# Kernel tuning notes

Hardware: AMD Instinct MI355X
Metric: run time of the kernel (lower is better)

## Reference

```python
import jax, jax.numpy as jnp
import numpy as np

DN = ('NCHW', 'OIHW', 'NCHW')

def _conv(x, w, b=None):
    # x: [P, C, H, W], w: [1, C, k, k] -> [P, 1, H, W] with SAME padding
    y = jax.lax.conv_general_dilated(x, w, (1, 1), 'SAME', dimension_numbers=DN)
    if b is not None:
        y = y + b[None, :, None, None]
    return y

def setup_inputs() -> dict:
    key = jax.random.key(0)
    ks = jax.random.split(key, 6)
    T, P, H, W = 36, 64, 128, 256
    K = 5
    inputs = jax.random.normal(ks[0], (T, P, H, W), dtype=jnp.float32)
    w_reset = 0.1 * jax.random.normal(ks[1], (1, 2, K, K), dtype=jnp.float32)
    b_reset = jnp.zeros((1,), dtype=jnp.float32)
    w_update = 0.1 * jax.random.normal(ks[2], (1, 2, K, K), dtype=jnp.float32)
    b_update = jnp.zeros((1,), dtype=jnp.float32)
    w_out = 0.1 * jax.random.normal(ks[3], (1, 2, K, K), dtype=jnp.float32)
    gam = jnp.ones((P,), dtype=jnp.float32)
    add_weights = 0.02 * jax.random.normal(ks[4], (P, H, W), dtype=jnp.float32)
    bias = jnp.zeros((H, W), dtype=jnp.float32)
    return {"inputs": inputs, "w_reset": w_reset, "b_reset": b_reset,
            "w_update": w_update, "b_update": b_update, "w_out": w_out,
            "gam": gam, "add_weights": add_weights, "bias": bias}

def reference(inputs, w_reset, b_reset, w_update, b_update, w_out, gam, add_weights, bias):
    # inputs: [T, P, H, W]; renormalize by per-plant scale gam
    x = gam[None, :, None, None] * inputs
    x = x[:, :, None]  # [T, P, 1, H, W] (channel dim = 1)
    h0 = jnp.zeros_like(x[0])  # [P, 1, H, W]

    def step(h, xt):
        stacked = jnp.concatenate([xt, h], axis=1)  # [P, 2, H, W]
        u = jax.nn.sigmoid(_conv(stacked, w_update, b_update))  # update gate
        r = jax.nn.sigmoid(_conv(stacked, w_reset, b_reset))    # reset gate
        c = _conv(jnp.concatenate([xt, r * h], axis=1), w_out)  # candidate (no bias, no act)
        h_new = h * (1.0 - u) + c * u
        return h_new, h_new

    _, states = jax.lax.scan(step, h0, x)  # [T, P, 1, H, W]
    s = states[:, :, 0]  # [T, P, H, W]
    # final layer (additive=False, rnn_act=None): tanh then per-plant spatial weights
    xs = jnp.tanh(s) * add_weights[None]
    out_y = xs.sum(axis=1) + bias[None]  # [T, H, W]
    return out_y, xs
```

## Files before the change

### kernel.cpp

```cpp
#include <hip/hip_runtime.h>

constexpr int T = 36, P = 64, H = 128, W = 256;
constexpr int HW  = H * W;
constexpr int PHW = P * HW;

constexpr int TH   = 16;
constexpr int NB   = 8;
constexpr int NBLK = P * NB;
constexpr int SR = 25, SC = 268;
constexpr int RR = 20;

constexpr long long TMO_ARRIVE = 3000000;
constexpr long long TMO_STEP   = 1000000;

typedef float vfloat4 __attribute__((ext_vector_type(4)));

__device__ __forceinline__ float fast_sigmoid(float z) {
    float e = __expf(-z);
    return __builtin_amdgcn_rcpf(1.0f + e);
}
__device__ __forceinline__ float fast_tanh(float x) {
    float e = __expf(-2.0f * fabsf(x));
    float t = (1.0f - e) * __builtin_amdgcn_rcpf(1.0f + e);
    return copysignf(t, x);
}

__device__ __forceinline__ void lds_store4(float* d, float4 v) {
    *(float2*)d       = make_float2(v.x, v.y);
    *(float2*)(d + 2) = make_float2(v.z, v.w);
}

__global__ __launch_bounds__(512, 4) void gru_all(
    const float* __restrict__ inputs, const float* __restrict__ gam,
    const float* __restrict__ w_update, const float* __restrict__ b_update,
    const float* __restrict__ w_reset,  const float* __restrict__ b_reset,
    const float* __restrict__ w_out,    const float* __restrict__ add_w,
    float* __restrict__ xs, float* __restrict__ hhalo, int* __restrict__ flags)
{
    __shared__ __align__(16) float sx[SR][SC];
    __shared__ __align__(16) float sh[SR][SC];
    __shared__ __align__(16) float srh[RR][SC];
    __shared__ int s_nowait;

    const int tid  = threadIdx.x;
    const int bid  = blockIdx.x;
    const int p    = bid >> 3;
    const int band = bid & 7;
    const int y0   = band * TH;

    const float gamma = gam[p];
    const float bu = b_update[0];
    const float br = b_reset[0];

    const int cg = tid & 63, rbb = tid >> 6;
    const int ox = 4 * cg,   oy  = 2 * rbb;

    int* flagsTop = flags;
    int* flagsBot = flags + NBLK;

    if (tid == 0) {
        s_nowait = 0;
        __hip_atomic_fetch_add(&flags[2 * NBLK], 1, __ATOMIC_RELAXED, __HIP_MEMORY_SCOPE_AGENT);
        const long long t0 = (long long)__builtin_amdgcn_s_memrealtime();
        while (__hip_atomic_load(&flags[2 * NBLK], __ATOMIC_RELAXED, __HIP_MEMORY_SCOPE_AGENT) < NBLK) {
            __builtin_amdgcn_s_sleep(16);
            if ((long long)__builtin_amdgcn_s_memrealtime() - t0 > TMO_ARRIVE) { s_nowait = 1; break; }
        }
    }

    float4 aw4[2];
    #pragma unroll
    for (int k = 0; k < 2; ++k)
        aw4[k] = *(const float4*)&add_w[(size_t)p * HW + (y0 + oy + k) * W + ox];

    for (int s = tid; s < SR * SC; s += 512) {
        (&sx[0][0])[s] = 0.f;
        (&sh[0][0])[s] = 0.f;
    }
    __syncthreads();
    {
        const float* xt = inputs + (size_t)p * HW;
        #pragma unroll
        for (int k = 0; k < 3; ++k) {
            const int s = tid + 512 * k;
            const int r = s >> 6, c4 = s & 63;
            const int gy = y0 + r - 4;
            if ((unsigned)gy < (unsigned)H) {
                float4 v = *(const float4*)&xt[gy * W + 4 * c4];
                v.x *= gamma; v.y *= gamma; v.z *= gamma; v.w *= gamma;
                lds_store4(&sx[r][6 + 4 * c4], v);
            }
        }
    }
    __syncthreads();

    #pragma unroll 1
    for (int t = 0; t < T; ++t) {
        if (tid < 462) {
            const int b  = tid / 66;
            const int g  = tid - 66 * b;
            const int r0 = 3 * b;
            const int c0 = 4 * g;
            float racc[3][4], hold[3][4];
            #pragma unroll
            for (int k = 0; k < 3; ++k)
                #pragma unroll
                for (int c = 0; c < 4; ++c) racc[k][c] = br;
            #pragma unroll
            for (int ir = 0; ir < 7; ++ir) {
                const float4 xa = *(const float4*)&sx[r0 + ir][c0];
                const float4 xb = *(const float4*)&sx[r0 + ir][c0 + 4];
                const float4 ha = *(const float4*)&sh[r0 + ir][c0];
                const float4 hb = *(const float4*)&sh[r0 + ir][c0 + 4];
                const float vx[8] = {xa.x, xa.y, xa.z, xa.w, xb.x, xb.y, xb.z, xb.w};
                const float vh[8] = {ha.x, ha.y, ha.z, ha.w, hb.x, hb.y, hb.z, hb.w};
                if (ir >= 2 && ir <= 4) {
                    #pragma unroll
                    for (int c = 0; c < 4; ++c) hold[ir - 2][c] = vh[c + 2];
                }
                #pragma unroll
                for (int k = 0; k < 3; ++k) {
                    const int dy = ir - k;
                    if (dy >= 0 && dy <= 4) {
                        #pragma unroll
                        for (int dx = 0; dx < 5; ++dx) {
                            const float wx = w_reset[dy * 5 + dx];
                            const float wh = w_reset[25 + dy * 5 + dx];
                            #pragma unroll
                            for (int c = 0; c < 4; ++c) {
                                racc[k][c] = fmaf(vx[c + dx], wx, racc[k][c]);
                                racc[k][c] = fmaf(vh[c + dx], wh, racc[k][c]);
                            }
                        }
                    }
                }
            }
            #pragma unroll
            for (int k = 0; k < 3; ++k) {
                if (r0 + k < RR) {
                    float4 v;
                    v.x = fast_sigmoid(racc[k][0]) * hold[k][0];
                    v.y = fast_sigmoid(racc[k][1]) * hold[k][1];
                    v.z = fast_sigmoid(racc[k][2]) * hold[k][2];
                    v.w = fast_sigmoid(racc[k][3]) * hold[k][3];
                    lds_store4(&srh[r0 + k][c0 + 2], v);
                }
            }
        }
        __syncthreads();

        float4 hn4[2];
        {
            float uacc[2][4], cacc[2][4], hold[2][4];
            #pragma unroll
            for (int k = 0; k < 2; ++k)
                #pragma unroll
                for (int c = 0; c < 4; ++c) { uacc[k][c] = bu; cacc[k][c] = 0.f; }
            #pragma unroll
            for (int ir = 0; ir < 6; ++ir) {
                const int sr = oy + 2 + ir;
                const float4 xa = *(const float4*)&sx[sr][ox + 4];
                const float4 xb = *(const float4*)&sx[sr][ox + 8];
                const float4 ha = *(const float4*)&sh[sr][ox + 4];
                const float4 hb = *(const float4*)&sh[sr][ox + 8];
                const float4 ra = *(const float4*)&srh[oy + ir][ox + 4];
                const float4 rb = *(const float4*)&srh[oy + ir][ox + 8];
                const float vx[8] = {xa.x, xa.y, xa.z, xa.w, xb.x, xb.y, xb.z, xb.w};
                const float vh[8] = {ha.x, ha.y, ha.z, ha.w, hb.x, hb.y, hb.z, hb.w};
                const float vr[8] = {ra.x, ra.y, ra.z, ra.w, rb.x, rb.y, rb.z, rb.w};
                if (ir == 2) {
                    #pragma unroll
                    for (int c = 0; c < 4; ++c) hold[0][c] = vh[c + 2];
                }
                if (ir == 3) {
                    #pragma unroll
                    for (int c = 0; c < 4; ++c) hold[1][c] = vh[c + 2];
                }
                #pragma unroll
                for (int k = 0; k < 2; ++k) {
                    const int dy = ir - k;
                    if (dy >= 0 && dy <= 4) {
                        #pragma unroll
                        for (int dx = 0; dx < 5; ++dx) {
                            const float wux = w_update[dy * 5 + dx];
                            const float wuh = w_update[25 + dy * 5 + dx];
                            const float wox = w_out[dy * 5 + dx];
                            const float wor = w_out[25 + dy * 5 + dx];
                            #pragma unroll
                            for (int c = 0; c < 4; ++c) {
                                uacc[k][c] = fmaf(vx[c + dx], wux, uacc[k][c]);
                                uacc[k][c] = fmaf(vh[c + dx], wuh, uacc[k][c]);
                                cacc[k][c] = fmaf(vx[c + dx], wox, cacc[k][c]);
                                cacc[k][c] = fmaf(vr[c + dx], wor, cacc[k][c]);
                            }
                        }
                    }
                }
            }
            #pragma unroll
            for (int k = 0; k < 2; ++k) {
                float hn[4];
                #pragma unroll
                for (int c = 0; c < 4; ++c) {
                    const float u = fast_sigmoid(uacc[k][c]);
                    hn[c] = hold[k][c] + (cacc[k][c] - hold[k][c]) * u;
                }
                hn4[k] = make_float4(hn[0], hn[1], hn[2], hn[3]);
            }
        }
        __syncthreads();

        if (t + 1 < T) {
            if (rbb < 2 && band > 0) {
                float* hb = hhalo + (size_t)(t & 1) * (NBLK * 2048) + (size_t)bid * 2048;
                #pragma unroll
                for (int k = 0; k < 2; ++k) {
                    float* d = &hb[(oy + k) * 256 + ox];
                    __hip_atomic_store(&d[0], hn4[k].x, __ATOMIC_RELAXED, __HIP_MEMORY_SCOPE_AGENT);
                    __hip_atomic_store(&d[1], hn4[k].y, __ATOMIC_RELAXED, __HIP_MEMORY_SCOPE_AGENT);
                    __hip_atomic_store(&d[2], hn4[k].z, __ATOMIC_RELAXED, __HIP_MEMORY_SCOPE_AGENT);
                    __hip_atomic_store(&d[3], hn4[k].w, __ATOMIC_RELAXED, __HIP_MEMORY_SCOPE_AGENT);
                }
                asm volatile("s_waitcnt vmcnt(0)" ::: "memory");
                if (cg == 0)
                    __hip_atomic_fetch_add(&flagsTop[bid], 1, __ATOMIC_RELAXED, __HIP_MEMORY_SCOPE_AGENT);
            }
            if (rbb >= 6 && band < 7) {
                float* hb = hhalo + (size_t)(t & 1) * (NBLK * 2048) + (size_t)bid * 2048;
                #pragma unroll
                for (int k = 0; k < 2; ++k) {
                    float* d = &hb[(oy + k - 8) * 256 + ox];
                    __hip_atomic_store(&d[0], hn4[k].x, __ATOMIC_RELAXED, __HIP_MEMORY_SCOPE_AGENT);
                    __hip_atomic_store(&d[1], hn4[k].y, __ATOMIC_RELAXED, __HIP_MEMORY_SCOPE_AGENT);
                    __hip_atomic_store(&d[2], hn4[k].z, __ATOMIC_RELAXED, __HIP_MEMORY_SCOPE_AGENT);
                    __hip_atomic_store(&d[3], hn4[k].w, __ATOMIC_RELAXED, __HIP_MEMORY_SCOPE_AGENT);
                }
                asm volatile("s_waitcnt vmcnt(0)" ::: "memory");
                if (cg == 0)
                    __hip_atomic_fetch_add(&flagsBot[bid], 1, __ATOMIC_RELAXED, __HIP_MEMORY_SCOPE_AGENT);
            }
        }

        #pragma unroll
        for (int k = 0; k < 2; ++k)
            lds_store4(&sh[4 + oy + k][6 + ox], hn4[k]);
        if (t + 1 < T) {
            const float* xt = inputs + (size_t)(t + 1) * PHW + (size_t)p * HW;
            #pragma unroll
            for (int k = 0; k < 3; ++k) {
                const int s = tid + 512 * k;
                const int r = s >> 6, c4 = s & 63;
                const int gy = y0 + r - 4;
                if ((unsigned)gy < (unsigned)H) {
                    float4 v = *(const float4*)&xt[gy * W + 4 * c4];
                    v.x *= gamma; v.y *= gamma; v.z *= gamma; v.w *= gamma;
                    lds_store4(&sx[r][6 + 4 * c4], v);
                }
            }
        }
        {
            float* xso = xs + (size_t)t * PHW + (size_t)p * HW;
            #pragma unroll
            for (int k = 0; k < 2; ++k) {
                vfloat4 v;
                v.x = fast_tanh(hn4[k].x) * aw4[k].x;
                v.y = fast_tanh(hn4[k].y) * aw4[k].y;
                v.z = fast_tanh(hn4[k].z) * aw4[k].z;
                v.w = fast_tanh(hn4[k].w) * aw4[k].w;
                __builtin_nontemporal_store(v, (vfloat4*)&xso[(y0 + oy + k) * W + ox]);
            }
        }
        if (t + 1 >= T) break;

        if (tid == 0 && band > 0 && !s_nowait) {
            const long long t0 = (long long)__builtin_amdgcn_s_memrealtime();
            while (__hip_atomic_load(&flagsBot[bid - 1], __ATOMIC_RELAXED, __HIP_MEMORY_SCOPE_AGENT) < 2 * (t + 1)) {
                __builtin_amdgcn_s_sleep(1);
                if ((long long)__builtin_amdgcn_s_memrealtime() - t0 > TMO_STEP) { s_nowait = 1; break; }
            }
        }
        if (tid == 64 && band < 7 && !s_nowait) {
            const long long t0 = (long long)__builtin_amdgcn_s_memrealtime();
            while (__hip_atomic_load(&flagsTop[bid + 1], __ATOMIC_RELAXED, __HIP_MEMORY_SCOPE_AGENT) < 2 * (t + 1)) {
                __builtin_amdgcn_s_sleep(1);
                if ((long long)__builtin_amdgcn_s_memrealtime() - t0 > TMO_STEP) { s_nowait = 1; break; }
            }
        }
        __syncthreads();

        {
            float* hb0 = hhalo + (size_t)(t & 1) * (NBLK * 2048);
            const int r = tid >> 6, c4 = tid & 63;
            if (r < 4) {
                if (band > 0) {
                    float* src = &hb0[(size_t)(bid - 1) * 2048 + (4 + r) * 256 + 4 * c4];
                    float4 v;
                    v.x = __hip_atomic_load(&src[0], __ATOMIC_RELAXED, __HIP_MEMORY_SCOPE_AGENT);
                    v.y = __hip_atomic_load(&src[1], __ATOMIC_RELAXED, __HIP_MEMORY_SCOPE_AGENT);
                    v.z = __hip_atomic_load(&src[2], __ATOMIC_RELAXED, __HIP_MEMORY_SCOPE_AGENT);
                    v.w = __hip_atomic_load(&src[3], __ATOMIC_RELAXED, __HIP_MEMORY_SCOPE_AGENT);
                    lds_store4(&sh[r][6 + 4 * c4], v);
                }
            } else {
                if (band < 7) {
                    float* src = &hb0[(size_t)(bid + 1) * 2048 + (r - 4) * 256 + 4 * c4];
                    float4 v;
                    v.x = __hip_atomic_load(&src[0], __ATOMIC_RELAXED, __HIP_MEMORY_SCOPE_AGENT);
                    v.y = __hip_atomic_load(&src[1], __ATOMIC_RELAXED, __HIP_MEMORY_SCOPE_AGENT);
                    v.z = __hip_atomic_load(&src[2], __ATOMIC_RELAXED, __HIP_MEMORY_SCOPE_AGENT);
                    v.w = __hip_atomic_load(&src[3], __ATOMIC_RELAXED, __HIP_MEMORY_SCOPE_AGENT);
                    lds_store4(&sh[16 + r][6 + 4 * c4], v);
                }
            }
        }
        __syncthreads();
    }
}

__global__ __launch_bounds__(256) void reduce_out(
    const float* __restrict__ xs, const float* __restrict__ bias,
    float* __restrict__ out_y)
{
    const int i4  = blockIdx.x * 256 + threadIdx.x;
    const int t   = i4 / (HW / 4);
    const int yx4 = i4 - t * (HW / 4);
    const float4* __restrict__ src = (const float4*)(xs + (size_t)t * PHW) + yx4;
    const float4  b4 = ((const float4*)bias)[yx4];
    float a0[4] = {b4.x, b4.y, b4.z, b4.w};
    float a1[4] = {0.f, 0.f, 0.f, 0.f};
    #pragma unroll 8
    for (int p = 0; p < P; p += 2) {
        const float4 v0 = src[(size_t)p * (HW / 4)];
        const float4 v1 = src[(size_t)(p + 1) * (HW / 4)];
        a0[0] += v0.x; a0[1] += v0.y; a0[2] += v0.z; a0[3] += v0.w;
        a1[0] += v1.x; a1[1] += v1.y; a1[2] += v1.z; a1[3] += v1.w;
    }
    ((float4*)out_y)[i4] = make_float4(a0[0] + a1[0], a0[1] + a1[1],
                                       a0[2] + a1[2], a0[3] + a1[3]);
}

extern "C" void kernel_launch(void* const* d_in, const int* in_sizes, int n_in,
                              void* d_out, int out_size, void* d_ws, size_t ws_size,
                              hipStream_t stream) {
    const float* inputs   = (const float*)d_in[0];
    const float* w_reset  = (const float*)d_in[1];
    const float* b_reset  = (const float*)d_in[2];
    const float* w_update = (const float*)d_in[3];
    const float* b_update = (const float*)d_in[4];
    const float* w_out    = (const float*)d_in[5];
    const float* gam      = (const float*)d_in[6];
    const float* add_w    = (const float*)d_in[7];
    const float* bias     = (const float*)d_in[8];

    float* out_y = (float*)d_out;
    float* xs    = out_y + (size_t)T * HW;

    float* hhalo = (float*)d_ws;
    int*   flags = (int*)((char*)d_ws + (size_t)2 * NBLK * 2048 * sizeof(float));

    (void)hipMemsetAsync(flags, 0, (2 * NBLK + 1) * sizeof(int), stream);

    gru_all<<<dim3(NBLK), dim3(512), 0, stream>>>(
        inputs, gam, w_update, b_update, w_reset, b_reset, w_out, add_w,
        xs, hhalo, flags);

    const int nout4 = T * HW / 4;
    reduce_out<<<nout4 / 256, 256, 0, stream>>>(xs, bias, out_y);
}
```

Before: 773.9 us.

## Overlap halo exchange with reset-gate conv via dedicated wave and LDS flag

Drops the end-of-step neighbor wait, barrier and halo load. Wave 7 now spins on the neighbor flags and fetches the halo rows at the start of the next step, while waves 2-4 start the reset-gate convolution on interior rows. Waves that need halo rows spin on an LDS ready counter instead. The next-step input prefetch is issued into registers before the xs stores and written to LDS afterward, hiding global load latency. This risks LDS spin-wait overhead, and the remapped phase-1 work leaves wave 7 carrying extra slots.

```diff
diff --git a/kernel.cpp b/kernel.cpp
--- a/kernel.cpp
+++ b/kernel.cpp
@@ -41,6 +41,7 @@
     __shared__ __align__(16) float sh[SR][SC];
     __shared__ __align__(16) float srh[RR][SC];
     __shared__ int s_nowait;
+    __shared__ int s_haloready;
 
     const int tid  = threadIdx.x;
     const int bid  = blockIdx.x;
@@ -52,14 +53,15 @@
     const float bu = b_update[0];
     const float br = b_reset[0];
 
-    const int cg = tid & 63, rbb = tid >> 6;
-    const int ox = 4 * cg,   oy  = 2 * rbb;
+    const int lane = tid & 63, rbb = tid >> 6;
+    const int ox = 4 * lane, oy = 2 * rbb;
 
     int* flagsTop = flags;
     int* flagsBot = flags + NBLK;
 
     if (tid == 0) {
         s_nowait = 0;
+        s_haloready = 0;
         __hip_atomic_fetch_add(&flags[2 * NBLK], 1, __ATOMIC_RELAXED, __HIP_MEMORY_SCOPE_AGENT);
         const long long t0 = (long long)__builtin_amdgcn_s_memrealtime();
         while (__hip_atomic_load(&flags[2 * NBLK], __ATOMIC_RELAXED, __HIP_MEMORY_SCOPE_AGENT) < NBLK) {
@@ -94,58 +96,113 @@
     }
     __syncthreads();
 
+    auto ph1_slot = [&](int b, int g) {
+        const int r0 = 3 * b;
+        const int c0 = 4 * g;
+        float racc[3][4], hold[3][4];
+        #pragma unroll
+        for (int k = 0; k < 3; ++k)
+            #pragma unroll
+            for (int c = 0; c < 4; ++c) racc[k][c] = br;
+        #pragma unroll
+        for (int ir = 0; ir < 7; ++ir) {
+            const float4 xa = *(const float4*)&sx[r0 + ir][c0];
+            const float4 xb = *(const float4*)&sx[r0 + ir][c0 + 4];
+            const float4 ha = *(const float4*)&sh[r0 + ir][c0];
+            const float4 hb = *(const float4*)&sh[r0 + ir][c0 + 4];
+            const float vx[8] = {xa.x, xa.y, xa.z, xa.w, xb.x, xb.y, xb.z, xb.w};
+            const float vh[8] = {ha.x, ha.y, ha.z, ha.w, hb.x, hb.y, hb.z, hb.w};
+            if (ir >= 2 && ir <= 4) {
+                #pragma unroll
+                for (int c = 0; c < 4; ++c) hold[ir - 2][c] = vh[c + 2];
+            }
+            #pragma unroll
+            for (int k = 0; k < 3; ++k) {
+                const int dy = ir - k;
+                if (dy >= 0 && dy <= 4) {
+                    #pragma unroll
+                    for (int dx = 0; dx < 5; ++dx) {
+                        const float wx = w_reset[dy * 5 + dx];
+                        const float wh = w_reset[25 + dy * 5 + dx];
+                        #pragma unroll
+                        for (int c = 0; c < 4; ++c) {
+                            racc[k][c] = fmaf(vx[c + dx], wx, racc[k][c]);
+                            racc[k][c] = fmaf(vh[c + dx], wh, racc[k][c]);
+                        }
+                    }
+                }
+            }
+        }
+        #pragma unroll
+        for (int k = 0; k < 3; ++k) {
+            if (r0 + k < RR) {
+                float4 v;
+                v.x = fast_sigmoid(racc[k][0]) * hold[k][0];
+                v.y = fast_sigmoid(racc[k][1]) * hold[k][1];
+                v.z = fast_sigmoid(racc[k][2]) * hold[k][2];
+                v.w = fast_sigmoid(racc[k][3]) * hold[k][3];
+                lds_store4(&srh[r0 + k][c0 + 2], v);
+            }
+        }
+    };
+
     #pragma unroll 1
     for (int t = 0; t < T; ++t) {
-        if (tid < 462) {
-            const int b  = tid / 66;
-            const int g  = tid - 66 * b;
-            const int r0 = 3 * b;
-            const int c0 = 4 * g;
-            float racc[3][4], hold[3][4];
-            #pragma unroll
-            for (int k = 0; k < 3; ++k)
-                #pragma unroll
-                for (int c = 0; c < 4; ++c) racc[k][c] = br;
-            #pragma unroll
-            for (int ir = 0; ir < 7; ++ir) {
-                const float4 xa = *(const float4*)&sx[r0 + ir][c0];
-                const float4 xb = *(const float4*)&sx[r0 + ir][c0 + 4];
-                const float4 ha = *(const float4*)&sh[r0 + ir][c0];
-                const float4 hb = *(const float4*)&sh[r0 + ir][c0 + 4];
-                const float vx[8] = {xa.x, xa.y, xa.z, xa.w, xb.x, xb.y, xb.z, xb.w};
-                const float vh[8] = {ha.x, ha.y, ha.z, ha.w, hb.x, hb.y, hb.z, hb.w};
-                if (ir >= 2 && ir <= 4) {
+        if (rbb < 7) {
+            if (t > 0 && (rbb == 0 || rbb == 1 || rbb == 5 || rbb == 6)) {
+                while (__hip_atomic_load(&s_haloready, __ATOMIC_ACQUIRE, __HIP_MEMORY_SCOPE_WORKGROUP) < t)
+                    __builtin_amdgcn_s_sleep(1);
+            }
+            ph1_slot(rbb, lane);
+        } else {
+            if (t > 0) {
+                if (lane == 0 && !s_nowait) {
+                    const long long t0 = (long long)__builtin_amdgcn_s_memrealtime();
+                    if (band > 0) {
+                        while (__hip_atomic_load(&flagsBot[bid - 1], __ATOMIC_RELAXED, __HIP_MEMORY_SCOPE_AGENT) < 2 * t) {
+                            __builtin_amdgcn_s_sleep(1);
+                            if ((long long)__builtin_amdgcn_s_memrealtime() - t0 > TMO_STEP) { s_nowait = 1; break; }
+                        }
+                    }
+                    if (band < 7) {
+                        while (__hip_atomic_load(&flagsTop[bid + 1], __ATOMIC_RELAXED, __HIP_MEMORY_SCOPE_AGENT) < 2 * t) {
+                            __builtin_amdgcn_s_sleep(1);
+                            if ((long long)__builtin_amdgcn_s_memrealtime() - t0 > TMO_STEP) { s_nowait = 1; break; }
+                        }
+                    }
+                }
+                {
+                    float* hb0 = hhalo + (size_t)((t - 1) & 1) * (NBLK * 2048);
                     #pragma unroll
-                    for (int c = 0; c < 4; ++c) hold[ir - 2][c] = vh[c + 2];
-                }
-                #pragma unroll
-                for (int k = 0; k < 3; ++k) {
-                    const int dy = ir - k;
-                    if (dy >= 0 && dy <= 4) {
-                        #pragma unroll
-                        for (int dx = 0; dx < 5; ++dx) {
-                            const float wx = w_reset[dy * 5 + dx];
-                            const float wh = w_reset[25 + dy * 5 + dx];
-                            #pragma unroll
-                            for (int c = 0; c < 4; ++c) {
-                                racc[k][c] = fmaf(vx[c + dx], wx, racc[k][c]);
-                                racc[k][c] = fmaf(vh[c + dx], wh, racc[k][c]);
+                    for (int r = 0; r < 8; ++r) {
+                        if (r < 4) {
+                            if (band > 0) {
+                                float* src = &hb0[(size_t)(bid - 1) * 2048 + (4 + r) * 256 + 4 * lane];
+                                float4 v;
+                                v.x = __hip_atomic_load(&src[0], __ATOMIC_RELAXED, __HIP_MEMORY_SCOPE_AGENT);
+                                v.y = __hip_atomic_load(&src[1], __ATOMIC_RELAXED, __HIP_MEMORY_SCOPE_AGENT);
+                                v.z = __hip_atomic_load(&src[2], __ATOMIC_RELAXED, __HIP_MEMORY_SCOPE_AGENT);
+                                v.w = __hip_atomic_load(&src[3], __ATOMIC_RELAXED, __HIP_MEMORY_SCOPE_AGENT);
+                                lds_store4(&sh[r][6 + 4 * lane], v);
                             }
-                        }
-                    }
-                }
-            }
-            #pragma unroll
-            for (int k = 0; k < 3; ++k) {
-                if (r0 + k < RR) {
-                    float4 v;
-                    v.x = fast_sigmoid(racc[k][0]) * hold[k][0];
-                    v.y = fast_sigmoid(racc[k][1]) * hold[k][1];
-                    v.z = fast_sigmoid(racc[k][2]) * hold[k][2];
-                    v.w = fast_sigmoid(racc[k][3]) * hold[k][3];
-                    lds_store4(&srh[r0 + k][c0 + 2], v);
-                }
-            }
+                        } else {
+                            if (band < 7) {
+                                float* src = &hb0[(size_t)(bid + 1) * 2048 + (r - 4) * 256 + 4 * lane];
+                                float4 v;
+                                v.x = __hip_atomic_load(&src[0], __ATOMIC_RELAXED, __HIP_MEMORY_SCOPE_AGENT);
+                                v.y = __hip_atomic_load(&src[1], __ATOMIC_RELAXED, __HIP_MEMORY_SCOPE_AGENT);
+                                v.z = __hip_atomic_load(&src[2], __ATOMIC_RELAXED, __HIP_MEMORY_SCOPE_AGENT);
+                                v.w = __hip_atomic_load(&src[3], __ATOMIC_RELAXED, __HIP_MEMORY_SCOPE_AGENT);
+                                lds_store4(&sh[16 + r][6 + 4 * lane], v);
+                            }
+                        }
+                    }
+                }
+                asm volatile("s_waitcnt lgkmcnt(0)" ::: "memory");
+                if (lane == 0)
+                    __hip_atomic_store(&s_haloready, t, __ATOMIC_RELEASE, __HIP_MEMORY_SCOPE_WORKGROUP);
+            }
+            if (lane < 14) ph1_slot(lane >> 1, 64 + (lane & 1));
         }
         __syncthreads();
 
@@ -222,7 +279,7 @@
                     __hip_atomic_store(&d[3], hn4[k].w, __ATOMIC_RELAXED, __HIP_MEMORY_SCOPE_AGENT);
                 }
                 asm volatile("s_waitcnt vmcnt(0)" ::: "memory");
-                if (cg == 0)
+                if (lane == 0)
                     __hip_atomic_fetch_add(&flagsTop[bid], 1, __ATOMIC_RELAXED, __HIP_MEMORY_SCOPE_AGENT);
             }
             if (rbb >= 6 && band < 7) {
@@ -236,14 +293,12 @@
                     __hip_atomic_store(&d[3], hn4[k].w, __ATOMIC_RELAXED, __HIP_MEMORY_SCOPE_AGENT);
                 }
                 asm volatile("s_waitcnt vmcnt(0)" ::: "memory");
-                if (cg == 0)
+                if (lane == 0)
                     __hip_atomic_fetch_add(&flagsBot[bid], 1, __ATOMIC_RELAXED, __HIP_MEMORY_SCOPE_AGENT);
             }
         }
 
-        #pragma unroll
-        for (int k = 0; k < 2; ++k)
-            lds_store4(&sh[4 + oy + k][6 + ox], hn4[k]);
+        float4 xp[3];
         if (t + 1 < T) {
             const float* xt = inputs + (size_t)(t + 1) * PHW + (size_t)p * HW;
             #pragma unroll
@@ -251,12 +306,13 @@
                 const int s = tid + 512 * k;
                 const int r = s >> 6, c4 = s & 63;
                 const int gy = y0 + r - 4;
-                if ((unsigned)gy < (unsigned)H) {
-                    float4 v = *(const float4*)&xt[gy * W + 4 * c4];
-                    v.x *= gamma; v.y *= gamma; v.z *= gamma; v.w *= gamma;
-                    lds_store4(&sx[r][6 + 4 * c4], v);
-                }
-            }
+                xp[k] = make_float4(0.f, 0.f, 0.f, 0.f);
+                if ((unsigned)gy < (unsigned)H)
+                    xp[k] = *(const float4*)&xt[gy * W + 4 * c4];
+            }
+            #pragma unroll
+            for (int k = 0; k < 2; ++k)
+                lds_store4(&sh[4 + oy + k][6 + ox], hn4[k]);
         }
         {
             float* xso = xs + (size_t)t * PHW + (size_t)p * HW;
@@ -271,45 +327,16 @@
             }
         }
         if (t + 1 >= T) break;
-
-        if (tid == 0 && band > 0 && !s_nowait) {
-            const long long t0 = (long long)__builtin_amdgcn_s_memrealtime();
-            while (__hip_atomic_load(&flagsBot[bid - 1], __ATOMIC_RELAXED, __HIP_MEMORY_SCOPE_AGENT) < 2 * (t + 1)) {
-                __builtin_amdgcn_s_sleep(1);
-                if ((long long)__builtin_amdgcn_s_memrealtime() - t0 > TMO_STEP) { s_nowait = 1; break; }
-            }
-        }
-        if (tid == 64 && band < 7 && !s_nowait) {
-            const long long t0 = (long long)__builtin_amdgcn_s_memrealtime();
-            while (__hip_atomic_load(&flagsTop[bid + 1], __ATOMIC_RELAXED, __HIP_MEMORY_SCOPE_AGENT) < 2 * (t + 1)) {
-                __builtin_amdgcn_s_sleep(1);
-                if ((long long)__builtin_amdgcn_s_memrealtime() - t0 > TMO_STEP) { s_nowait = 1; break; }
-            }
-        }
-        __syncthreads();
-
         {
-            float* hb0 = hhalo + (size_t)(t & 1) * (NBLK * 2048);
-            const int r = tid >> 6, c4 = tid & 63;
-            if (r < 4) {
-                if (band > 0) {
-                    float* src = &hb0[(size_t)(bid - 1) * 2048 + (4 + r) * 256 + 4 * c4];
-                    float4 v;
-                    v.x = __hip_atomic_load(&src[0], __ATOMIC_RELAXED, __HIP_MEMORY_SCOPE_AGENT);
-                    v.y = __hip_atomic_load(&src[1], __ATOMIC_RELAXED, __HIP_MEMORY_SCOPE_AGENT);
-                    v.z = __hip_atomic_load(&src[2], __ATOMIC_RELAXED, __HIP_MEMORY_SCOPE_AGENT);
-                    v.w = __hip_atomic_load(&src[3], __ATOMIC_RELAXED, __HIP_MEMORY_SCOPE_AGENT);
-                    lds_store4(&sh[r][6 + 4 * c4], v);
-                }
-            } else {
-                if (band < 7) {
-                    float* src = &hb0[(size_t)(bid + 1) * 2048 + (r - 4) * 256 + 4 * c4];
-                    float4 v;
-                    v.x = __hip_atomic_load(&src[0], __ATOMIC_RELAXED, __HIP_MEMORY_SCOPE_AGENT);
-                    v.y = __hip_atomic_load(&src[1], __ATOMIC_RELAXED, __HIP_MEMORY_SCOPE_AGENT);
-                    v.z = __hip_atomic_load(&src[2], __ATOMIC_RELAXED, __HIP_MEMORY_SCOPE_AGENT);
-                    v.w = __hip_atomic_load(&src[3], __ATOMIC_RELAXED, __HIP_MEMORY_SCOPE_AGENT);
-                    lds_store4(&sh[16 + r][6 + 4 * c4], v);
+            #pragma unroll
+            for (int k = 0; k < 3; ++k) {
+                const int s = tid + 512 * k;
+                const int r = s >> 6, c4 = s & 63;
+                const int gy = y0 + r - 4;
+                if ((unsigned)gy < (unsigned)H) {
+                    float4 v = xp[k];
+                    v.x *= gamma; v.y *= gamma; v.z *= gamma; v.w *= gamma;
+                    lds_store4(&sx[r][6 + 4 * c4], v);
                 }
             }
         }
```

After: 967.6 us. +25.0%, slower.
